# Kernel optimization log

Hardware: AMD Instinct MI355X
Metric: run time of the kernel (lower is better)

The kernel has to match this reference:

```python
import jax, jax.numpy as jnp
import numpy as np

TEMP = 0.5   # temperature from __init__
EPS = 1e-8   # torch.nn.CosineSimilarity eps


def setup_inputs() -> dict:
    key = jax.random.key(0)
    N, D = 8192, 256
    x = jax.random.normal(key, (N, D), dtype=jnp.float32)
    # pairs: each label appears exactly twice, as required for the
    # sim[~mask].reshape(N, -1) in the original to be well-formed
    y = jnp.arange(N, dtype=jnp.int32) // 2
    return {"x": x, "y": y}


def reference(x, y):
    # cosine similarity matrix: normalize once, then one NxD @ DxN matmul
    # (equivalent to CosineSimilarity(x.unsqueeze(1), x.unsqueeze(0)) without
    #  the NxNxD intermediate)
    norm = jnp.maximum(jnp.linalg.norm(x, axis=1, keepdims=True), EPS)
    xn = x / norm
    sim = (xn @ xn.T) / TEMP                     # [N, N]

    # Original: positives = equal-label entries (row-major order, includes the
    # diagonal), logits = [positives | negatives] which is just a per-row
    # permutation of sim; labels = 0 -> CE target is the FIRST equal-label
    # column of each row. logsumexp is over the full row (all N entries).
    eq = y[:, None] == y[None, :]                # [N, N] bool
    first_pos = jnp.argmax(eq, axis=1)           # first column j with y_j == y_i
    target = jnp.take_along_axis(sim, first_pos[:, None], axis=1)[:, 0]  # [N]

    lse = jax.nn.logsumexp(sim, axis=1)          # [N]
    N = x.shape[0]
    loss = jnp.sum(lse - target) / N             # CrossEntropyLoss(sum) / N
    return loss
```

## Files before the change

kernel.cpp:

```cpp
#include <hip/hip_runtime.h>
#include <hip/hip_bf16.h>

#define D 256
#define INV_TEMP 2.0f

typedef __attribute__((ext_vector_type(8))) short short8;
typedef __attribute__((ext_vector_type(4))) float floatx4;

__device__ __forceinline__ unsigned short f2bf(float f) {
    union { float f; unsigned u; } a; a.f = f;
    unsigned r = (a.u + 0x7fffu + ((a.u >> 16) & 1u)) >> 16;
    return (unsigned short)r;
}

__global__ void nt_prep_kernel(const float* __restrict__ x,
                               unsigned short* __restrict__ xnb,
                               float* __restrict__ pair_dot) {
    int p    = blockIdx.x * 4 + (threadIdx.x >> 6);
    int lane = threadIdx.x & 63;
    const float4* a4 = (const float4*)(x + (size_t)(2 * p) * D);
    const float4* b4 = (const float4*)(x + (size_t)(2 * p + 1) * D);
    float4 a = a4[lane], b = b4[lane];
    float saa = a.x * a.x + a.y * a.y + a.z * a.z + a.w * a.w;
    float sbb = b.x * b.x + b.y * b.y + b.z * b.z + b.w * b.w;
    float sab = a.x * b.x + a.y * b.y + a.z * b.z + a.w * b.w;
    #pragma unroll
    for (int off = 32; off; off >>= 1) {
        saa += __shfl_xor(saa, off);
        sbb += __shfl_xor(sbb, off);
        sab += __shfl_xor(sab, off);
    }
    float inva = 1.0f / fmaxf(sqrtf(saa), 1e-8f);
    float invb = 1.0f / fmaxf(sqrtf(sbb), 1e-8f);
    ushort4 oa, ob;
    oa.x = f2bf(a.x * inva); oa.y = f2bf(a.y * inva);
    oa.z = f2bf(a.z * inva); oa.w = f2bf(a.w * inva);
    ob.x = f2bf(b.x * invb); ob.y = f2bf(b.y * invb);
    ob.z = f2bf(b.z * invb); ob.w = f2bf(b.w * invb);
    ((ushort4*)(xnb + (size_t)(2 * p) * D))[lane] = oa;
    ((ushort4*)(xnb + (size_t)(2 * p + 1) * D))[lane] = ob;
    if (lane == 0)
        pair_dot[p] = sab * inva * invb * INV_TEMP;
}

__global__ __launch_bounds__(256)
void nt_simexp_kernel(const unsigned short* __restrict__ xnb,
                      float* __restrict__ contrib) {
    __shared__ __align__(16) unsigned short As[2][128 * 64];
    __shared__ __align__(16) unsigned short Bs[2][128 * 64];

    int idx = blockIdx.x;
    int bi = (int)((sqrtf(8.0f * (float)idx + 1.0f) - 1.0f) * 0.5f);
    while ((bi + 1) * (bi + 2) / 2 <= idx) ++bi;
    while (bi * (bi + 1) / 2 > idx) --bi;
    int bj = idx - bi * (bi + 1) / 2;

    const int rowA0 = bi * 128, rowB0 = bj * 128;
    const bool diag = (bi == bj);

    const int tid  = threadIdx.x;
    const int wave = tid >> 6, lane = tid & 63;
    const int wm   = wave & 1, wn = wave >> 1;
    const int quad = lane >> 4, c = lane & 15;

    const unsigned short* Ag = xnb + (size_t)rowA0 * D;
    const unsigned short* Bg = xnb + (size_t)rowB0 * D;

    auto ldtile = [&](const unsigned short* src, int k0, uint4* r4) {
        #pragma unroll
        for (int it = 0; it < 4; ++it) {
            int ci = it * 256 + tid, rr = ci >> 3, ch = ci & 7;
            r4[it] = *(const uint4*)(src + (size_t)rr * D + k0 + ch * 8);
        }
    };
    auto sttile = [&](unsigned short* dst, const uint4* r4) {
        #pragma unroll
        for (int it = 0; it < 4; ++it) {
            int ci = it * 256 + tid, rr = ci >> 3, ch = ci & 7;
            *(uint4*)(dst + rr * 64 + ((ch ^ (rr & 7)) * 8)) = r4[it];
        }
    };

    floatx4 acc[4][4];
    #pragma unroll
    for (int mt = 0; mt < 4; ++mt)
        #pragma unroll
        for (int nt = 0; nt < 4; ++nt)
            acc[mt][nt] = (floatx4){0.f, 0.f, 0.f, 0.f};

    auto compute = [&](const unsigned short* Ab, const unsigned short* Bb) {
        #pragma unroll
        for (int kk = 0; kk < 64; kk += 32) {
            short8 af[4], bf[4];
            #pragma unroll
            for (int mt = 0; mt < 4; ++mt) {
                int tr = wm * 64 + mt * 16 + c;
                int pp = ((kk >> 3) + quad) ^ (c & 7);
                af[mt] = *(const short8*)(Ab + tr * 64 + pp * 8);
            }
            #pragma unroll
            for (int nt = 0; nt < 4; ++nt) {
                int tr = wn * 64 + nt * 16 + c;
                int pp = ((kk >> 3) + quad) ^ (c & 7);
                bf[nt] = *(const short8*)(Bb + tr * 64 + pp * 8);
            }
            #pragma unroll
            for (int mt = 0; mt < 4; ++mt)
                #pragma unroll
                for (int nt = 0; nt < 4; ++nt)
                    acc[mt][nt] = __builtin_amdgcn_mfma_f32_16x16x32_bf16(
                        af[mt], bf[nt], acc[mt][nt], 0, 0, 0);
        }
    };

    {
        uint4 ra[4], rb[4];
        ldtile(Ag, 0, ra);
        if (!diag) ldtile(Bg, 0, rb);
        sttile(As[0], ra);
        if (!diag) sttile(Bs[0], rb);
    }
    __syncthreads();

    #pragma unroll
    for (int k = 0; k < 4; ++k) {
        const int cur = k & 1, nxt = cur ^ 1;
        uint4 ra[4], rb[4];
        if (k < 3) {
            ldtile(Ag, (k + 1) * 64, ra);
            if (!diag) ldtile(Bg, (k + 1) * 64, rb);
        }
        compute(As[cur], diag ? As[cur] : Bs[cur]);
        if (k < 3) {
            sttile(As[nxt], ra);
            if (!diag) sttile(Bs[nxt], rb);
            __syncthreads();
        }
    }

    #pragma unroll
    for (int mt = 0; mt < 4; ++mt)
        #pragma unroll
        for (int nt = 0; nt < 4; ++nt)
            #pragma unroll
            for (int r = 0; r < 4; ++r)
                acc[mt][nt][r] = __expf(acc[mt][nt][r] * INV_TEMP);

    float* smf = (float*)&As[0][0];

    #pragma unroll
    for (int mt = 0; mt < 4; ++mt) {
        float ps[4] = {0.f, 0.f, 0.f, 0.f};
        #pragma unroll
        for (int nt = 0; nt < 4; ++nt)
            #pragma unroll
            for (int r = 0; r < 4; ++r)
                ps[r] += acc[mt][nt][r];
        #pragma unroll
        for (int off = 1; off < 16; off <<= 1)
            #pragma unroll
            for (int r = 0; r < 4; ++r)
                ps[r] += __shfl_xor(ps[r], off);
        if (c == 0) {
            int rl = wm * 64 + mt * 16 + quad * 4;
            #pragma unroll
            for (int r = 0; r < 4; ++r)
                smf[wn * 128 + rl + r] = ps[r];
        }
    }
    if (!diag) {
        #pragma unroll
        for (int nt = 0; nt < 4; ++nt) {
            float cs = 0.f;
            #pragma unroll
            for (int mt = 0; mt < 4; ++mt)
                #pragma unroll
                for (int r = 0; r < 4; ++r)
                    cs += acc[mt][nt][r];
            cs += __shfl_xor(cs, 16);
            cs += __shfl_xor(cs, 32);
            if (quad == 0)
                smf[256 + wm * 128 + wn * 64 + nt * 16 + c] = cs;
        }
    }
    __syncthreads();

    if (tid < 128)
        contrib[((size_t)bi * 64 + bj) * 128 + tid] = smf[tid] + smf[128 + tid];
    else if (!diag) {
        int cl = tid - 128;
        contrib[((size_t)bj * 64 + bi) * 128 + cl] =
            smf[256 + cl] + smf[256 + 128 + cl];
    }
}

__global__ void nt_reduce_kernel(const float* __restrict__ contrib,
                                 const float* __restrict__ pair_dot,
                                 float* __restrict__ blockPart) {
    __shared__ float sm[256];
    int b  = blockIdx.x;
    int rl = threadIdx.x & 127, h = threadIdx.x >> 7;
    float s = 0.f;
    const float* base = contrib + ((size_t)b * 64 + h * 32) * 128 + rl;
    #pragma unroll
    for (int j = 0; j < 32; ++j) s += base[(size_t)j * 128];
    sm[threadIdx.x] = s;
    __syncthreads();
    float v = 0.f;
    if (h == 0) v = logf(sm[rl] + sm[128 + rl]);
    else if (rl < 64) v = -pair_dot[b * 64 + rl];
    __syncthreads();
    sm[threadIdx.x] = v;
    __syncthreads();
    for (int st = 128; st; st >>= 1) {
        if ((int)threadIdx.x < st) sm[threadIdx.x] += sm[threadIdx.x + st];
        __syncthreads();
    }
    if (threadIdx.x == 0) blockPart[b] = sm[0];
}

__global__ void nt_final_kernel(const float* __restrict__ blockPart,
                                float* __restrict__ out, int N) {
    int lane = threadIdx.x & 63;
    float s = blockPart[lane];
    #pragma unroll
    for (int off = 32; off; off >>= 1) s += __shfl_xor(s, off);
    if (lane == 0) out[0] = (s - (float)N) / (float)N;
}

extern "C" void kernel_launch(void* const* d_in, const int* in_sizes, int n_in,
                              void* d_out, int out_size, void* d_ws, size_t ws_size,
                              hipStream_t stream) {
    const float* x = (const float*)d_in[0];
    int N = in_sizes[0] / D;

    char* ws = (char*)d_ws;
    unsigned short* xnb = (unsigned short*)ws;
    float* pair_dot  = (float*)(ws + (size_t)N * D * 2);
    float* contrib   = pair_dot + N / 2;
    float* blockPart = contrib + 64 * 64 * 128;

    nt_prep_kernel<<<N / 8, 256, 0, stream>>>(x, xnb, pair_dot);
    int nb = (N / 128) * (N / 128 + 1) / 2;
    nt_simexp_kernel<<<nb, 256, 0, stream>>>(xnb, contrib);
    nt_reduce_kernel<<<N / 128, 256, 0, stream>>>(contrib, pair_dot, blockPart);
    nt_final_kernel<<<1, 64, 0, stream>>>(blockPart, (float*)d_out, N);
}
```

Before: 117.5 us.

## Persistent triangle-tiled simexp kernel with resident B panel and direct-to-LDS loads

Replaces the one-block-per-tile triangular launch with 256 persistent blocks. Each block walks a paired column strip (p and 63-p) so the work is balanced, and keeps the full-K B panel resident in LDS across the tiles of a strip. A tiles are double-buffered in K halves and loaded with global_load_lds straight into swizzled LDS, skipping the register staging. Partial row and column sums now go directly to global memory split per wave half, which doubles the contrib buffer and the reduce kernel's read loop. The cost is heavier LDS use (one block per CU) and less occupancy to hide latency.

```diff
diff --git a/kernel.cpp b/kernel.cpp
--- a/kernel.cpp
+++ b/kernel.cpp
@@ -11,6 +11,13 @@
     union { float f; unsigned u; } a; a.f = f;
     unsigned r = (a.u + 0x7fffu + ((a.u >> 16) & 1u)) >> 16;
     return (unsigned short)r;
+}
+
+__device__ __forceinline__ void gload_lds16(const unsigned short* g,
+                                            unsigned short* l) {
+    __builtin_amdgcn_global_load_lds(
+        (const __attribute__((address_space(1))) unsigned int*)g,
+        (__attribute__((address_space(3))) unsigned int*)l, 16, 0, 0);
 }
 
 __global__ void nt_prep_kernel(const float* __restrict__ x,
@@ -43,67 +50,63 @@
         pair_dot[p] = sab * inva * invb * INV_TEMP;
 }
 
-__global__ __launch_bounds__(256)
+__global__ __launch_bounds__(256, 1)
 void nt_simexp_kernel(const unsigned short* __restrict__ xnb,
                       float* __restrict__ contrib) {
-    __shared__ __align__(16) unsigned short As[2][128 * 64];
-    __shared__ __align__(16) unsigned short Bs[2][128 * 64];
-
-    int idx = blockIdx.x;
-    int bi = (int)((sqrtf(8.0f * (float)idx + 1.0f) - 1.0f) * 0.5f);
-    while ((bi + 1) * (bi + 2) / 2 <= idx) ++bi;
-    while (bi * (bi + 1) / 2 > idx) --bi;
-    int bj = idx - bi * (bi + 1) / 2;
-
-    const int rowA0 = bi * 128, rowB0 = bj * 128;
-    const bool diag = (bi == bj);
+    __shared__ __align__(16) unsigned short Bs[128 * 256];
+    __shared__ __align__(16) unsigned short As[2][128 * 128];
+
+    const int p = blockIdx.x >> 3, q = blockIdx.x & 7;
+    const int n1 = 64 - p;
 
     const int tid  = threadIdx.x;
     const int wave = tid >> 6, lane = tid & 63;
     const int wm   = wave & 1, wn = wave >> 1;
     const int quad = lane >> 4, c = lane & 15;
 
-    const unsigned short* Ag = xnb + (size_t)rowA0 * D;
-    const unsigned short* Bg = xnb + (size_t)rowB0 * D;
-
-    auto ldtile = [&](const unsigned short* src, int k0, uint4* r4) {
-        #pragma unroll
-        for (int it = 0; it < 4; ++it) {
-            int ci = it * 256 + tid, rr = ci >> 3, ch = ci & 7;
-            r4[it] = *(const uint4*)(src + (size_t)rr * D + k0 + ch * 8);
-        }
-    };
-    auto sttile = [&](unsigned short* dst, const uint4* r4) {
-        #pragma unroll
-        for (int it = 0; it < 4; ++it) {
-            int ci = it * 256 + tid, rr = ci >> 3, ch = ci & 7;
-            *(uint4*)(dst + rr * 64 + ((ch ^ (rr & 7)) * 8)) = r4[it];
+    auto tile_of = [&](int i, int& bi, int& bj) {
+        if (i < n1) { bi = p + i;      bj = p; }
+        else        { bi = 63 - p + (i - n1); bj = 63 - p; }
+    };
+
+    auto load_B = [&](int bj) {
+        const unsigned short* src = xnb + (size_t)(bj * 128) * D;
+        int rsub = lane >> 5, pp = lane & 31;
+        #pragma unroll
+        for (int t = 0; t < 16; ++t) {
+            int wl = wave * 16 + t;
+            int rr = wl * 2 + rsub;
+            int j  = (pp & ~7) | ((pp ^ rr) & 7);
+            gload_lds16(src + (size_t)rr * D + j * 8, Bs + wl * 512 + lane * 8);
+        }
+    };
+    auto load_A = [&](int bi, int kb, unsigned short* Ab) {
+        const unsigned short* src = xnb + (size_t)(bi * 128) * D + kb * 128;
+        int rsub = lane >> 4, pp = lane & 15;
+        #pragma unroll
+        for (int t = 0; t < 8; ++t) {
+            int wl = wave * 8 + t;
+            int rr = wl * 4 + rsub;
+            int jl = (pp & 8) | ((pp ^ rr) & 7);
+            gload_lds16(src + (size_t)rr * D + jl * 8, Ab + wl * 512 + lane * 8);
         }
     };
 
     floatx4 acc[4][4];
-    #pragma unroll
-    for (int mt = 0; mt < 4; ++mt)
-        #pragma unroll
-        for (int nt = 0; nt < 4; ++nt)
-            acc[mt][nt] = (floatx4){0.f, 0.f, 0.f, 0.f};
-
-    auto compute = [&](const unsigned short* Ab, const unsigned short* Bb) {
-        #pragma unroll
-        for (int kk = 0; kk < 64; kk += 32) {
+    auto compute = [&](const unsigned short* Ab, int kb) {
+        #pragma unroll
+        for (int kl = 0; kl < 4; ++kl) {
+            int jl = kl * 4 + quad;
+            int pA = (jl & 8) | ((jl ^ c) & 7);
+            int jg = kb * 16 + jl;
+            int pB = (jg & ~7) | ((jg ^ c) & 7);
             short8 af[4], bf[4];
             #pragma unroll
-            for (int mt = 0; mt < 4; ++mt) {
-                int tr = wm * 64 + mt * 16 + c;
-                int pp = ((kk >> 3) + quad) ^ (c & 7);
-                af[mt] = *(const short8*)(Ab + tr * 64 + pp * 8);
-            }
-            #pragma unroll
-            for (int nt = 0; nt < 4; ++nt) {
-                int tr = wn * 64 + nt * 16 + c;
-                int pp = ((kk >> 3) + quad) ^ (c & 7);
-                bf[nt] = *(const short8*)(Bb + tr * 64 + pp * 8);
-            }
+            for (int mt = 0; mt < 4; ++mt)
+                af[mt] = *(const short8*)(Ab + (wm * 64 + mt * 16 + c) * 128 + pA * 8);
+            #pragma unroll
+            for (int nt = 0; nt < 4; ++nt)
+                bf[nt] = *(const short8*)(Bs + (wn * 64 + nt * 16 + c) * 256 + pB * 8);
             #pragma unroll
             for (int mt = 0; mt < 4; ++mt)
                 #pragma unroll
@@ -113,84 +116,81 @@
         }
     };
 
-    {
-        uint4 ra[4], rb[4];
-        ldtile(Ag, 0, ra);
-        if (!diag) ldtile(Bg, 0, rb);
-        sttile(As[0], ra);
-        if (!diag) sttile(Bs[0], rb);
-    }
-    __syncthreads();
-
-    #pragma unroll
-    for (int k = 0; k < 4; ++k) {
-        const int cur = k & 1, nxt = cur ^ 1;
-        uint4 ra[4], rb[4];
-        if (k < 3) {
-            ldtile(Ag, (k + 1) * 64, ra);
-            if (!diag) ldtile(Bg, (k + 1) * 64, rb);
-        }
-        compute(As[cur], diag ? As[cur] : Bs[cur]);
-        if (k < 3) {
-            sttile(As[nxt], ra);
-            if (!diag) sttile(Bs[nxt], rb);
+    const int m = (q == 0) ? 9 : 8;
+    int bi, bj;
+    tile_of(q, bi, bj);
+    load_B(bj);
+    load_A(bi, 0, As[0]);
+    __syncthreads();
+
+    for (int j = 0; j < m; ++j) {
+        tile_of(q + 8 * j, bi, bj);
+        bool have_next = (j + 1 < m);
+        int nbi = 0, nbj = 0;
+        if (have_next) tile_of(q + 8 * (j + 1), nbi, nbj);
+        bool same = have_next && (nbj == bj);
+
+        #pragma unroll
+        for (int mt = 0; mt < 4; ++mt)
+            #pragma unroll
+            for (int nt = 0; nt < 4; ++nt)
+                acc[mt][nt] = (floatx4){0.f, 0.f, 0.f, 0.f};
+
+        load_A(bi, 1, As[1]);
+        compute(As[0], 0);
+        __syncthreads();
+        if (same) load_A(nbi, 0, As[0]);
+        compute(As[1], 1);
+
+        #pragma unroll
+        for (int mt = 0; mt < 4; ++mt)
+            #pragma unroll
+            for (int nt = 0; nt < 4; ++nt)
+                #pragma unroll
+                for (int r = 0; r < 4; ++r)
+                    acc[mt][nt][r] = __expf(acc[mt][nt][r] * INV_TEMP);
+
+        #pragma unroll
+        for (int mt = 0; mt < 4; ++mt) {
+            float ps[4] = {0.f, 0.f, 0.f, 0.f};
+            #pragma unroll
+            for (int nt = 0; nt < 4; ++nt)
+                #pragma unroll
+                for (int r = 0; r < 4; ++r)
+                    ps[r] += acc[mt][nt][r];
+            #pragma unroll
+            for (int off = 1; off < 16; off <<= 1)
+                #pragma unroll
+                for (int r = 0; r < 4; ++r)
+                    ps[r] += __shfl_xor(ps[r], off);
+            if (c == 0) {
+                float4 v = {ps[0], ps[1], ps[2], ps[3]};
+                *(float4*)(contrib + (((size_t)bi * 64 + bj) * 2 + wn) * 128 +
+                           wm * 64 + mt * 16 + quad * 4) = v;
+            }
+        }
+        if (bi != bj) {
+            #pragma unroll
+            for (int nt = 0; nt < 4; ++nt) {
+                float cs = 0.f;
+                #pragma unroll
+                for (int mt = 0; mt < 4; ++mt)
+                    #pragma unroll
+                    for (int r = 0; r < 4; ++r)
+                        cs += acc[mt][nt][r];
+                cs += __shfl_xor(cs, 16);
+                cs += __shfl_xor(cs, 32);
+                if (quad == 0)
+                    contrib[(((size_t)bj * 64 + bi) * 2 + wm) * 128 +
+                            wn * 64 + nt * 16 + c] = cs;
+            }
+        }
+        __syncthreads();
+        if (have_next && !same) {
+            load_B(nbj);
+            load_A(nbi, 0, As[0]);
             __syncthreads();
         }
-    }
-
-    #pragma unroll
-    for (int mt = 0; mt < 4; ++mt)
-        #pragma unroll
-        for (int nt = 0; nt < 4; ++nt)
-            #pragma unroll
-            for (int r = 0; r < 4; ++r)
-                acc[mt][nt][r] = __expf(acc[mt][nt][r] * INV_TEMP);
-
-    float* smf = (float*)&As[0][0];
-
-    #pragma unroll
-    for (int mt = 0; mt < 4; ++mt) {
-        float ps[4] = {0.f, 0.f, 0.f, 0.f};
-        #pragma unroll
-        for (int nt = 0; nt < 4; ++nt)
-            #pragma unroll
-            for (int r = 0; r < 4; ++r)
-                ps[r] += acc[mt][nt][r];
-        #pragma unroll
-        for (int off = 1; off < 16; off <<= 1)
-            #pragma unroll
-            for (int r = 0; r < 4; ++r)
-                ps[r] += __shfl_xor(ps[r], off);
-        if (c == 0) {
-            int rl = wm * 64 + mt * 16 + quad * 4;
-            #pragma unroll
-            for (int r = 0; r < 4; ++r)
-                smf[wn * 128 + rl + r] = ps[r];
-        }
-    }
-    if (!diag) {
-        #pragma unroll
-        for (int nt = 0; nt < 4; ++nt) {
-            float cs = 0.f;
-            #pragma unroll
-            for (int mt = 0; mt < 4; ++mt)
-                #pragma unroll
-                for (int r = 0; r < 4; ++r)
-                    cs += acc[mt][nt][r];
-            cs += __shfl_xor(cs, 16);
-            cs += __shfl_xor(cs, 32);
-            if (quad == 0)
-                smf[256 + wm * 128 + wn * 64 + nt * 16 + c] = cs;
-        }
-    }
-    __syncthreads();
-
-    if (tid < 128)
-        contrib[((size_t)bi * 64 + bj) * 128 + tid] = smf[tid] + smf[128 + tid];
-    else if (!diag) {
-        int cl = tid - 128;
-        contrib[((size_t)bj * 64 + bi) * 128 + cl] =
-            smf[256 + cl] + smf[256 + 128 + cl];
     }
 }
 
@@ -201,9 +201,9 @@
     int b  = blockIdx.x;
     int rl = threadIdx.x & 127, h = threadIdx.x >> 7;
     float s = 0.f;
-    const float* base = contrib + ((size_t)b * 64 + h * 32) * 128 + rl;
+    const float* base = contrib + (((size_t)b * 64) * 2 + h) * 128 + rl;
     #pragma unroll
-    for (int j = 0; j < 32; ++j) s += base[(size_t)j * 128];
+    for (int j = 0; j < 64; ++j) s += base[(size_t)j * 256];
     sm[threadIdx.x] = s;
     __syncthreads();
     float v = 0.f;
@@ -238,11 +238,10 @@
     unsigned short* xnb = (unsigned short*)ws;
     float* pair_dot  = (float*)(ws + (size_t)N * D * 2);
     float* contrib   = pair_dot + N / 2;
-    float* blockPart = contrib + 64 * 64 * 128;
+    float* blockPart = contrib + (size_t)64 * 64 * 2 * 128;
 
     nt_prep_kernel<<<N / 8, 256, 0, stream>>>(x, xnb, pair_dot);
-    int nb = (N / 128) * (N / 128 + 1) / 2;
-    nt_simexp_kernel<<<nb, 256, 0, stream>>>(xnb, contrib);
+    nt_simexp_kernel<<<256, 256, 0, stream>>>(xnb, contrib);
     nt_reduce_kernel<<<N / 128, 256, 0, stream>>>(contrib, pair_dot, blockPart);
     nt_final_kernel<<<1, 64, 0, stream>>>(blockPart, (float*)d_out, N);
 }
```

Result: faster. 107.5 us (-8.6%).
